# Performance work log

Measured on AMD Instinct MI355X. Metric: run time of the kernel, lower is better.

The kernel has to match this reference:

```python
import jax, jax.numpy as jnp
import numpy as np


def setup_inputs() -> dict:
    key = jax.random.key(0)
    k1, k2 = jax.random.split(key)
    B, L, E, K = 4, 1024, 512, 8
    xsa = jax.random.normal(k1, (B, L, E), dtype=jnp.float32)
    # attq.weight, torch Linear layout (out_features=K*E, in_features=E); scaled like a trained init
    Wq = jax.random.normal(k2, (K * E, E), dtype=jnp.float32) * 0.02
    return {"xsa": xsa, "Wq": Wq}


def reference(xsa, Wq):
    # xsa: (B, L, E); Wq: (K*E, E). attq bias, attk, and bias layers are unused in the original forward.
    B, L, E = xsa.shape
    K = Wq.shape[0] // E
    q = (xsa @ Wq.T).reshape(B, L, K, E)            # (B, L, K, E)
    # hijk = q @ xsa^T over E, per batch: (B, L, K, L)
    hijk = jnp.einsum('blke,bme->blkm', q, xsa) * (1.0 / (E ** 0.5))
    pijk = jax.nn.softmax(hijk, axis=-1)            # (B, L, K, L)
    yik = jnp.einsum('blkm,bme->blke', pijk, xsa)   # (B, L, K, E)  xsa doubles as V
    xid = yik.reshape(B, L, K * E)
    return (xid, pijk)
```

## Files before the change

### kernel.cpp

```cpp
#include <hip/hip_runtime.h>
#include <cstdint>
#include <cstddef>


typedef __bf16 bf16x8 __attribute__((ext_vector_type(8)));
typedef float f32x4 __attribute__((ext_vector_type(4)));

__device__ __forceinline__ unsigned short f2bf(float f) {
  union { float f; unsigned int u; } x; x.f = f;
  unsigned int u = x.u;
  unsigned int r = (u + 0x7fffu + ((u >> 16) & 1u)) >> 16;
  return (unsigned short)r;
}

__device__ __forceinline__ float bf2f(unsigned short s) {
  union { unsigned int u; float f; } x; x.u = ((unsigned int)s) << 16;
  return x.f;
}

__device__ __forceinline__ void async_cp16(const void* g, void* l) {
  __builtin_amdgcn_global_load_lds(
      (const __attribute__((address_space(1))) void*)g,
      (__attribute__((address_space(3))) void*)l, 16, 0, 0);
}

__device__ __forceinline__ void barrier_raw() {
  asm volatile("" ::: "memory");
  __builtin_amdgcn_s_barrier();
  asm volatile("" ::: "memory");
}

template <int MODE>
__global__ __launch_bounds__(512, 2) void gemm_nt256(
    const unsigned short* __restrict__ A, const unsigned short* __restrict__ Bt,
    void* __restrict__ Cv, float* __restrict__ sums, float* __restrict__ Pout,
    int M, int N, int Kd, size_t sA, size_t sB, size_t sC, float scale) {
  __shared__ __align__(16) unsigned short smem[2 * 2 * 256 * 64];

  const int tid  = threadIdx.x;
  const int lane = tid & 63;
  const int wave = tid >> 6;
  const int wm   = (wave >> 2) * 128;
  const int wn   = (wave & 3) * 64;
  const int quad = lane >> 4;
  const int lrow = lane & 15;

  const int m0 = blockIdx.x * 256;
  const int n0 = blockIdx.y * 256;
  const int b  = blockIdx.z;

  const unsigned short* Ab = A + (size_t)b * sA;
  const unsigned short* Bb = Bt + (size_t)b * sB;

  const int arow = lane >> 3;
  const int acb  = (lane & 7) ^ arow;
  const unsigned short* pA[4];
  const unsigned short* pB[4];
#pragma unroll
  for (int i = 0; i < 4; ++i) {
    const int c = i * 8 + wave;
    pA[i] = Ab + (size_t)(m0 + c * 8 + arow) * Kd + acb * 8;
    pB[i] = Bb + (size_t)(n0 + c * 8 + arow) * Kd + acb * 8;
  }

  auto stageA = [&](unsigned short* dst, int k0) {
#pragma unroll
    for (int i = 0; i < 4; ++i)
      async_cp16(pA[i] + k0, dst + (i * 8 + wave) * 512);
  };
  auto stageB = [&](unsigned short* dst, int k0) {
#pragma unroll
    for (int i = 0; i < 4; ++i)
      async_cp16(pB[i] + k0, dst + (i * 8 + wave) * 512);
  };

  float pinv[4];
  if constexpr (MODE == 2) {
#pragma unroll
    for (int p = 0; p < 4; ++p)
      pinv[p] = 1.0f / sums[(size_t)b * M + m0 + p * 64 + (tid >> 3)];
  }

  const int xo0 = ((0 + quad) ^ (lrow & 7)) << 3;
  const int xo1 = ((4 + quad) ^ (lrow & 7)) << 3;

  f32x4 acc[8][4];
#pragma unroll
  for (int i = 0; i < 8; ++i)
#pragma unroll
    for (int j = 0; j < 4; ++j) acc[i][j] = (f32x4){0.f, 0.f, 0.f, 0.f};

  bf16x8 a[4][2];
  bf16x8 bb[4][2];

  auto rdA = [&](int mq, const unsigned short* As_) {
#pragma unroll
    for (int f = 0; f < 4; ++f) {
      const int r = wm + mq * 64 + f * 16 + lrow;
      a[f][0] = *(const bf16x8*)&As_[r * 64 + xo0];
      a[f][1] = *(const bf16x8*)&As_[r * 64 + xo1];
    }
  };
  auto rdB = [&](int nq, const unsigned short* Bs_) {
#pragma unroll
    for (int f = 0; f < 2; ++f) {
      const int r = wn + nq * 32 + f * 16 + lrow;
      bb[nq * 2 + f][0] = *(const bf16x8*)&Bs_[r * 64 + xo0];
      bb[nq * 2 + f][1] = *(const bf16x8*)&Bs_[r * 64 + xo1];
    }
  };
  auto mm = [&](int mq, int nq) {
    __builtin_amdgcn_s_setprio(1);
#pragma unroll
    for (int ks = 0; ks < 2; ++ks)
#pragma unroll
      for (int f = 0; f < 4; ++f)
#pragma unroll
        for (int g = 0; g < 2; ++g)
          acc[mq * 4 + f][nq * 2 + g] = __builtin_amdgcn_mfma_f32_16x16x32_bf16(
              a[f][ks], bb[nq * 2 + g][ks], acc[mq * 4 + f][nq * 2 + g], 0, 0, 0);
    __builtin_amdgcn_s_setprio(0);
  };

  stageA(smem, 0);
  stageB(smem + 16384, 0);
  asm volatile("s_waitcnt vmcnt(0)" ::: "memory");
  barrier_raw();

  const int nt = Kd >> 6;
  for (int t = 0; t < nt; ++t) {
    const int cur = t & 1;
    const unsigned short* As_ = smem + cur * 32768;
    const unsigned short* Bs_ = As_ + 16384;
    unsigned short* An  = smem + ((cur ^ 1) * 32768);
    unsigned short* Bn_ = An + 16384;
    const bool pf = (t + 1 < nt);
    const int k1 = (t + 1) << 6;

    rdA(0, As_);
    rdB(0, Bs_);
    if (pf) stageA(An, k1);
    if constexpr (MODE == 2) {
      if ((t >> 3) == (int)blockIdx.y) {
        const int er = tid >> 3;
        const int cb = tid & 7;
#pragma unroll
        for (int p = 0; p < 4; ++p) {
          const int r = p * 64 + er;
          union { uint4 u; unsigned short s[8]; } v;
          v.u = *(const uint4*)(Ab + (size_t)(m0 + r) * Kd + t * 64 + cb * 8);
          float o[8];
#pragma unroll
          for (int u = 0; u < 8; ++u) o[u] = bf2f(v.s[u]) * pinv[p];
          float* dst = Pout + ((size_t)b * M + m0 + r) * (size_t)Kd + t * 64 + cb * 8;
          *(float4*)dst = *(float4*)&o[0];
          *(float4*)(dst + 4) = *(float4*)&o[4];
        }
      }
    }
    barrier_raw();
    mm(0, 0);
    barrier_raw();

    rdB(1, Bs_);
    if (pf) stageB(Bn_, k1);
    barrier_raw();
    mm(0, 1);
    barrier_raw();

    rdA(1, As_);
    barrier_raw();
    mm(1, 1);
    barrier_raw();

    mm(1, 0);
    asm volatile("s_waitcnt vmcnt(0)" ::: "memory");
    barrier_raw();
  }

  float* epi = (float*)smem;
  const int wmo = wm ? 16 : 0;
  const int erb = wmo + quad * 4;
#pragma unroll
  for (int fm = 0; fm < 8; ++fm) {
    float linv[4];
    if constexpr (MODE == 2) {
#pragma unroll
      for (int r = 0; r < 4; ++r)
        linv[r] = 1.0f / sums[(size_t)b * M + m0 + wm + fm * 16 + quad * 4 + r];
    }
    __syncthreads();
#pragma unroll
    for (int fn = 0; fn < 4; ++fn)
#pragma unroll
      for (int r = 0; r < 4; ++r) {
        float v = acc[fm][fn][r];
        if constexpr (MODE == 0) v *= scale;
        if constexpr (MODE == 1) v = __expf(v * scale);
        if constexpr (MODE == 2) v *= linv[r];
        epi[(erb + r) * 260 + wn + fn * 16 + lrow] = v;
      }
    __syncthreads();
#pragma unroll
    for (int rep = 0; rep < 4; ++rep) {
      const int lr = (tid >> 6) + rep * 8;
      const int gr = m0 + fm * 16 + (lr & 15) + (lr >= 16 ? 128 : 0);
      const int c4 = (tid & 63) * 4;
      float4 v4 = *(const float4*)&epi[lr * 260 + c4];
      if constexpr (MODE <= 1) {
        unsigned short* C = (unsigned short*)Cv + (size_t)b * sC;
        union { unsigned short s[4]; uint2 u; } pk;
        pk.s[0] = f2bf(v4.x); pk.s[1] = f2bf(v4.y);
        pk.s[2] = f2bf(v4.z); pk.s[3] = f2bf(v4.w);
        *(uint2*)&C[(size_t)gr * N + n0 + c4] = pk.u;
        if constexpr (MODE == 1) {
          float s = v4.x + v4.y + v4.z + v4.w;
          s += __shfl_xor(s, 1);
          s += __shfl_xor(s, 2);
          s += __shfl_xor(s, 4);
          s += __shfl_xor(s, 8);
          s += __shfl_xor(s, 16);
          s += __shfl_xor(s, 32);
          if (lane == 0) atomicAdd(&sums[(size_t)b * M + gr], s);
        }
      } else {
        float* C = (float*)Cv + (size_t)b * sC;
        *(float4*)&C[(size_t)gr * N + n0 + c4] = v4;
      }
    }
  }
}

__global__ __launch_bounds__(256) void cvt_f32_to_bf16(
    const float* __restrict__ in, unsigned short* __restrict__ out, int n4) {
  int i = blockIdx.x * blockDim.x + threadIdx.x;
  if (i < n4) {
    float4 v = *(const float4*)(in + (size_t)i * 4);
    union { unsigned short s[4]; uint2 v2; } pk;
    pk.s[0] = f2bf(v.x); pk.s[1] = f2bf(v.y);
    pk.s[2] = f2bf(v.z); pk.s[3] = f2bf(v.w);
    *(uint2*)(out + (size_t)i * 4) = pk.v2;
  }
}

__global__ __launch_bounds__(256) void cvt_and_transpose_bf16(
    const float* __restrict__ in, unsigned short* __restrict__ outS,
    unsigned short* __restrict__ outT, int L, int E) {
  __shared__ unsigned short tile[32][33];
  int b  = blockIdx.z;
  int e0 = blockIdx.x * 32;
  int l0 = blockIdx.y * 32;
  int tx = threadIdx.x & 31;
  int ty = threadIdx.x >> 5;
  const float* inb = in + (size_t)b * L * E;
  unsigned short* outSb = outS + (size_t)b * L * E;
#pragma unroll
  for (int r = 0; r < 32; r += 8) {
    unsigned short v = f2bf(inb[(size_t)(l0 + ty + r) * E + e0 + tx]);
    tile[ty + r][tx] = v;
    outSb[(size_t)(l0 + ty + r) * E + e0 + tx] = v;
  }
  __syncthreads();
  unsigned short* outTb = outT + (size_t)b * L * E;
#pragma unroll
  for (int r = 0; r < 32; r += 8)
    outTb[(size_t)(e0 + ty + r) * L + l0 + tx] = tile[tx][ty + r];
}

extern "C" void kernel_launch(void* const* d_in, const int* in_sizes, int n_in,
                              void* d_out, int out_size, void* d_ws, size_t ws_size,
                              hipStream_t stream) {
  const float* xsa = (const float*)d_in[0];
  const float* Wq  = (const float*)d_in[1];
  float* out = (float*)d_out;

  const int Bn = 4, L = 1024, E = 512, K = 8;
  const int M1 = Bn * L;
  const int N1 = K * E;
  const int M2 = L * K;
  const size_t xid_n = (size_t)Bn * L * K * E;

  float* xid  = out;
  float* pijk = out + xid_n;

  unsigned short* ws   = (unsigned short*)d_ws;
  unsigned short* WqB  = ws;
  unsigned short* xsaB = WqB + (size_t)N1 * E;
  unsigned short* xsaT = xsaB + (size_t)Bn * L * E;
  unsigned short* QB   = xsaT + (size_t)Bn * L * E;
  unsigned short* PuB  = QB + (size_t)M1 * N1;
  float* sums = (float*)(PuB + (size_t)Bn * M2 * L);

  {
    int n4 = (N1 * E) / 4;
    cvt_f32_to_bf16<<<dim3((n4 + 255) / 256), dim3(256), 0, stream>>>(Wq, WqB, n4);
    cvt_and_transpose_bf16<<<dim3(E / 32, L / 32, Bn), dim3(256), 0, stream>>>(
        xsa, xsaB, xsaT, L, E);
    hipMemsetAsync(sums, 0, (size_t)Bn * M2 * sizeof(float), stream);
  }

  gemm_nt256<0><<<dim3(M1 / 256, N1 / 256, 1), dim3(512), 0, stream>>>(
      xsaB, WqB, QB, nullptr, nullptr, M1, N1, E, 0, 0, 0, 1.0f);

  gemm_nt256<1><<<dim3(M2 / 256, L / 256, Bn), dim3(512), 0, stream>>>(
      QB, xsaB, PuB, sums, nullptr, M2, L, E,
      (size_t)M2 * E, (size_t)L * E, (size_t)M2 * L, 0.04419417382415922f);

  gemm_nt256<2><<<dim3(M2 / 256, E / 256, Bn), dim3(512), 0, stream>>>(
      PuB, xsaT, xid, sums, pijk, M2, E, L,
      (size_t)M2 * L, (size_t)E * L, (size_t)M2 * E, 1.0f);
}
```

Measured before the change: 325.4 us.

## Remove intra-iteration barriers in GEMM loop and fuse prep kernels into one launch

The GEMM main loop now issues async staging of both A and B for the next tile at the top of each iteration. It then does all LDS fragment reads and MFMAs without the intermediate barriers, keeping only the final vmcnt wait and one barrier per k-tile. Separately, the Wq bf16 conversion, the xsa convert-and-transpose, and the sums memset are merged into a single prep kernel that picks its role by block index. The aim is to cut barrier stalls and launch overhead. The cost is less explicit interleaving of memory and MFMA phases, which may affect how well LDS reads overlap with compute.

```diff
diff --git a/kernel.cpp b/kernel.cpp
--- a/kernel.cpp
+++ b/kernel.cpp
@@ -134,12 +134,12 @@
     const unsigned short* Bs_ = As_ + 16384;
     unsigned short* An  = smem + ((cur ^ 1) * 32768);
     unsigned short* Bn_ = An + 16384;
-    const bool pf = (t + 1 < nt);
-    const int k1 = (t + 1) << 6;
-
-    rdA(0, As_);
-    rdB(0, Bs_);
-    if (pf) stageA(An, k1);
+
+    if (t + 1 < nt) {
+      const int k1 = (t + 1) << 6;
+      stageA(An, k1);
+      stageB(Bn_, k1);
+    }
     if constexpr (MODE == 2) {
       if ((t >> 3) == (int)blockIdx.y) {
         const int er = tid >> 3;
@@ -158,21 +158,13 @@
         }
       }
     }
-    barrier_raw();
+    rdA(0, As_);
+    rdB(0, Bs_);
+    rdB(1, Bs_);
     mm(0, 0);
-    barrier_raw();
-
-    rdB(1, Bs_);
-    if (pf) stageB(Bn_, k1);
-    barrier_raw();
     mm(0, 1);
-    barrier_raw();
-
     rdA(1, As_);
-    barrier_raw();
     mm(1, 1);
-    barrier_raw();
-
     mm(1, 0);
     asm volatile("s_waitcnt vmcnt(0)" ::: "memory");
     barrier_raw();
@@ -231,29 +223,34 @@
   }
 }
 
-__global__ __launch_bounds__(256) void cvt_f32_to_bf16(
-    const float* __restrict__ in, unsigned short* __restrict__ out, int n4) {
-  int i = blockIdx.x * blockDim.x + threadIdx.x;
-  if (i < n4) {
-    float4 v = *(const float4*)(in + (size_t)i * 4);
-    union { unsigned short s[4]; uint2 v2; } pk;
-    pk.s[0] = f2bf(v.x); pk.s[1] = f2bf(v.y);
-    pk.s[2] = f2bf(v.z); pk.s[3] = f2bf(v.w);
-    *(uint2*)(out + (size_t)i * 4) = pk.v2;
-  }
-}
-
-__global__ __launch_bounds__(256) void cvt_and_transpose_bf16(
-    const float* __restrict__ in, unsigned short* __restrict__ outS,
-    unsigned short* __restrict__ outT, int L, int E) {
+__global__ __launch_bounds__(256) void prep(
+    const float* __restrict__ Wq, unsigned short* __restrict__ WqB,
+    const float* __restrict__ xsa, unsigned short* __restrict__ xsaB,
+    unsigned short* __restrict__ xsaT, float* __restrict__ sums,
+    int L, int E, int wq_n4, int sums_n4) {
+  const int bid = blockIdx.x;
+  if (bid < 64) {
+    const int gtid = bid * 256 + threadIdx.x;
+    for (int i = gtid; i < wq_n4; i += 64 * 256) {
+      float4 v = *(const float4*)(Wq + (size_t)i * 4);
+      union { unsigned short s[4]; uint2 v2; } pk;
+      pk.s[0] = f2bf(v.x); pk.s[1] = f2bf(v.y);
+      pk.s[2] = f2bf(v.z); pk.s[3] = f2bf(v.w);
+      *(uint2*)(WqB + (size_t)i * 4) = pk.v2;
+    }
+    if (gtid < sums_n4)
+      *(float4*)(sums + (size_t)gtid * 4) = (float4){0.f, 0.f, 0.f, 0.f};
+    return;
+  }
   __shared__ unsigned short tile[32][33];
-  int b  = blockIdx.z;
-  int e0 = blockIdx.x * 32;
-  int l0 = blockIdx.y * 32;
-  int tx = threadIdx.x & 31;
-  int ty = threadIdx.x >> 5;
-  const float* inb = in + (size_t)b * L * E;
-  unsigned short* outSb = outS + (size_t)b * L * E;
+  const int idx = bid - 64;
+  const int e0 = (idx & 15) * 32;
+  const int l0 = ((idx >> 4) & 31) * 32;
+  const int b  = idx >> 9;
+  const int tx = threadIdx.x & 31;
+  const int ty = threadIdx.x >> 5;
+  const float* inb = xsa + (size_t)b * L * E;
+  unsigned short* outSb = xsaB + (size_t)b * L * E;
 #pragma unroll
   for (int r = 0; r < 32; r += 8) {
     unsigned short v = f2bf(inb[(size_t)(l0 + ty + r) * E + e0 + tx]);
@@ -261,7 +258,7 @@
     outSb[(size_t)(l0 + ty + r) * E + e0 + tx] = v;
   }
   __syncthreads();
-  unsigned short* outTb = outT + (size_t)b * L * E;
+  unsigned short* outTb = xsaT + (size_t)b * L * E;
 #pragma unroll
   for (int r = 0; r < 32; r += 8)
     outTb[(size_t)(e0 + ty + r) * L + l0 + tx] = tile[tx][ty + r];
@@ -292,11 +289,10 @@
   float* sums = (float*)(PuB + (size_t)Bn * M2 * L);
 
   {
-    int n4 = (N1 * E) / 4;
-    cvt_f32_to_bf16<<<dim3((n4 + 255) / 256), dim3(256), 0, stream>>>(Wq, WqB, n4);
-    cvt_and_transpose_bf16<<<dim3(E / 32, L / 32, Bn), dim3(256), 0, stream>>>(
-        xsa, xsaB, xsaT, L, E);
-    hipMemsetAsync(sums, 0, (size_t)Bn * M2 * sizeof(float), stream);
+    const int wq_n4 = (N1 * E) / 4;
+    const int sums_n4 = (Bn * M2) / 4;
+    prep<<<dim3(64 + (E / 32) * (L / 32) * Bn), dim3(256), 0, stream>>>(
+        Wq, WqB, xsa, xsaB, xsaT, sums, L, E, wq_n4, sums_n4);
   }
 
   gemm_nt256<0><<<dim3(M1 / 256, N1 / 256, 1), dim3(512), 0, stream>>>(
```

Result: no change. 323.9 us (-0.5%).
